# Performance work log

Measured on AMD Instinct MI355X. Metric: run time of the kernel, lower is better.

The kernel has to match this reference:

```python
import jax, jax.numpy as jnp
import numpy as np

N_NODES = 50000
N_EDGES = 1600000
IN_F, H_F, N_C = 128, 128, 16
NEG_SLOPE = 0.2  # DGL GATConv default


def setup_inputs() -> dict:
    key = jax.random.key(0)
    ks = jax.random.split(key, 12)
    def w(k, shape, fan_in):
        return jax.random.normal(k, shape, jnp.float32) / np.float32(np.sqrt(fan_in))
    return {
        "feat": jax.random.normal(ks[0], (N_NODES, IN_F), jnp.float32),
        "src": jax.random.randint(ks[1], (N_EDGES,), 0, N_NODES, dtype=jnp.int32),
        "dst": jax.random.randint(ks[2], (N_EDGES,), 0, N_NODES, dtype=jnp.int32),
        "W1": w(ks[3], (IN_F, H_F), IN_F), "al1": w(ks[4], (H_F,), H_F), "ar1": w(ks[5], (H_F,), H_F), "b1": jnp.zeros((H_F,), jnp.float32),
        "W2": w(ks[6], (H_F, H_F), H_F), "al2": w(ks[7], (H_F,), H_F), "ar2": w(ks[8], (H_F,), H_F), "b2": jnp.zeros((H_F,), jnp.float32),
        "W3": w(ks[9], (H_F, N_C), H_F), "al3": w(ks[10], (N_C,), N_C), "ar3": w(ks[11], (N_C,), N_C), "b3": jnp.zeros((N_C,), jnp.float32),
    }


def _gat_layer(h, src, dst, W, al, ar, b):
    # DGL GATConv (1 head): ft = W h; e_ij = LeakyReLU(a_l.ft_src + a_r.ft_dst);
    # alpha = edge_softmax over incoming edges of dst; out = sum alpha * ft_src + bias
    ft = h @ W                                   # [N, out]
    el = ft @ al                                 # [N]
    er = ft @ ar                                 # [N]
    e = jax.nn.leaky_relu(el[src] + er[dst], negative_slope=NEG_SLOPE)  # [E]
    emax = jax.ops.segment_max(e, dst, num_segments=N_NODES)
    emax = jnp.where(jnp.isfinite(emax), emax, 0.0)  # guard isolated nodes
    ex = jnp.exp(e - emax[dst])                  # [E]
    esum = jax.ops.segment_sum(ex, dst, num_segments=N_NODES)  # [N]
    agg = jax.ops.segment_sum(ex[:, None] * ft[src], dst, num_segments=N_NODES)  # [N, out]
    out = agg / jnp.where(esum > 0, esum, 1.0)[:, None] + b
    return jax.nn.relu(out)


def reference(feat, src, dst, W1, al1, ar1, b1, W2, al2, ar2, b2, W3, al3, ar3, b3):
    h = _gat_layer(feat, src, dst, W1, al1, ar1, b1)
    h = _gat_layer(h, src, dst, W2, al2, ar2, b2)
    h = _gat_layer(h, src, dst, W3, al3, ar3, b3)
    return h  # [N_NODES, N_C]
```

## Files before the change

### kernel.cpp

```cpp
#include <hip/hip_runtime.h>
#include <hip/hip_bf16.h>

#define NN 50000
#define NE 1600000
#define FF 128
#define CC 16
#define NB ((NN + 63) / 64)
#define NBLK 128
#define CH ((NE + NBLK - 1) / NBLK)

using bf16 = __hip_bfloat16;
using bf16x8 = __attribute__((ext_vector_type(8))) short;
using f32x4  = __attribute__((ext_vector_type(4))) float;

static __device__ __forceinline__ float ldf(const void* p, int i, int isbf){
    return isbf ? __bfloat162float(((const bf16*)p)[i]) : ((const float*)p)[i];
}
static __device__ __forceinline__ float bflo(unsigned u){
    union{unsigned x; float f;} c; c.x = u << 16; return c.f;
}
static __device__ __forceinline__ float bfhi(unsigned u){
    union{unsigned x; float f;} c; c.x = u & 0xFFFF0000u; return c.f;
}
static __device__ __forceinline__ float rdlanef(float v, int l){
    return __int_as_float(__builtin_amdgcn_readlane(__float_as_int(v), l));
}
static __device__ __forceinline__ unsigned short f2bfu(float v){
    bf16 b = __float2bfloat16(v);
    union{bf16 b; unsigned short u;} c; c.b = b; return c.u;
}

__global__ __launch_bounds__(256) void k_detect(const unsigned short* __restrict__ u,
                                                int* __restrict__ flag){
    int t = threadIdx.x;
    unsigned short lo = u[2 * t];
    int e = (lo >> 7) & 0xFF;
    int sane = (e >= 117 && e <= 137) ? 1 : 0;
    __shared__ int cnt;
    if (t == 0) cnt = 0;
    __syncthreads();
    atomicAdd(&cnt, sane);
    __syncthreads();
    if (t == 0) *flag = (cnt >= 128) ? 1 : 0;
}

__global__ __launch_bounds__(256) void k_zero(int* __restrict__ p, int n){
    int i = blockIdx.x * 256 + threadIdx.x;
    if (i < n) p[i] = 0;
}

__global__ __launch_bounds__(256) void k_wprep(const void* __restrict__ W1, const void* __restrict__ W2,
                                               const int* __restrict__ dflag, unsigned short* __restrict__ wtg){
    const int isbf = *dflag;
    int idx = blockIdx.x * 256 + threadIdx.x;
    int l = idx >> 14;
    int e = idx & 16383;
    int f = e >> 7, k = e & 127;
    const void* W = l ? W2 : W1;
    wtg[idx] = f2bfu(ldf(W, k * FF + f, isbf));
}


__global__ __launch_bounds__(256) void k_bcount(const int* __restrict__ dst, int* __restrict__ bcounts,
                                                int* __restrict__ bh){
    __shared__ int hist[NB];
    const int t = threadIdx.x, b = blockIdx.x;
    for (int i = t; i < NB; i += 256) hist[i] = 0;
    __syncthreads();
    const int beg = b * CH, end = (beg + CH < NE) ? beg + CH : NE;
    for (int i = beg + t; i < end; i += 256){
        int d = dst[i];
        if ((unsigned)d >= NN) d = 0;
        atomicAdd(&hist[d >> 6], 1);
    }
    __syncthreads();
    for (int k = t; k < NB; k += 256){
        int v = hist[k];
        bh[k * NBLK + b] = v;
        if (v) atomicAdd(&bcounts[k], v);
    }
}

__global__ __launch_bounds__(256) void k_bscan(const int* __restrict__ bcounts, int* __restrict__ bbase,
                                               int* __restrict__ rowptr){
    __shared__ int s[256];
    const int t = threadIdx.x;
    constexpr int PT = (NB + 255) / 256;
    int loc[PT];
    int sum = 0;
    #pragma unroll
    for (int i = 0; i < PT; i++){
        int idx = t * PT + i;
        int v = (idx < NB) ? bcounts[idx] : 0;
        loc[i] = sum;
        sum += v;
    }
    s[t] = sum; __syncthreads();
    for (int off = 1; off < 256; off <<= 1){
        int x = (t >= off) ? s[t - off] : 0;
        __syncthreads();
        s[t] += x;
        __syncthreads();
    }
    int base = (t > 0) ? s[t - 1] : 0;
    #pragma unroll
    for (int i = 0; i < PT; i++){
        int idx = t * PT + i;
        if (idx < NB) bbase[idx] = base + loc[i];
    }
    if (t == 255){
        bbase[NB] = s[255];
        rowptr[NN] = s[255];
    }
}

__global__ __launch_bounds__(256) void k_boffset(const int* __restrict__ bbase, int* __restrict__ bh){
    int k = blockIdx.x * 4 + (threadIdx.x >> 6);
    int lane = threadIdx.x & 63;
    if (k >= NB) return;
    int v0 = bh[k * NBLK + 2 * lane];
    int v1 = bh[k * NBLK + 2 * lane + 1];
    int s = v0 + v1;
    #pragma unroll
    for (int off = 1; off < 64; off <<= 1){
        int x = __shfl_up(s, off);
        if (lane >= off) s += x;
    }
    int base = bbase[k] + s - (v0 + v1);
    bh[k * NBLK + 2 * lane]     = base;
    bh[k * NBLK + 2 * lane + 1] = base + v0;
}

__global__ __launch_bounds__(256) void k_bucket(const int* __restrict__ src, const int* __restrict__ dst,
                                                const int* __restrict__ bh, unsigned* __restrict__ bpairs){
    __shared__ int cur[NB];
    const int t = threadIdx.x, b = blockIdx.x;
    for (int k = t; k < NB; k += 256) cur[k] = bh[k * NBLK + b];
    __syncthreads();
    const int beg = b * CH, end = (beg + CH < NE) ? beg + CH : NE;
    for (int i = beg + t; i < end; i += 256){
        int s = src[i];
        int d = dst[i];
        if ((unsigned)s >= NN) s = 0;
        if ((unsigned)d >= NN) d = 0;
        int p = atomicAdd(&cur[d >> 6], 1);
        if ((unsigned)p < NE) bpairs[p] = (unsigned)s | ((unsigned)(d & 63) << 16);
    }
}

__global__ __launch_bounds__(256) void k_bsort(const unsigned* __restrict__ bpairs, const int* __restrict__ bbase,
                                               int* __restrict__ rowptr, int* __restrict__ csrsrc){
    __shared__ int cnt[64];
    __shared__ int cur[64];
    const int t = threadIdx.x;
    const int b = blockIdx.x;
    const int base = bbase[b];
    const int endb = bbase[b + 1];
    if (t < 64) cnt[t] = 0;
    __syncthreads();
    for (int i = base + t; i < endb; i += 256)
        atomicAdd(&cnt[bpairs[i] >> 16], 1);
    __syncthreads();
    if (t < 64){
        int v = cnt[t];
        int inc = v;
        #pragma unroll
        for (int off = 1; off < 64; off <<= 1){
            int x = __shfl_up(inc, off);
            if (t >= off) inc += x;
        }
        int excl = inc - v;
        cur[t] = excl;
        int d = b * 64 + t;
        if (d < NN) rowptr[d] = base + excl;
    }
    __syncthreads();
    for (int i = base + t; i < endb; i += 256){
        unsigned pr = bpairs[i];
        int p = atomicAdd(&cur[pr >> 16], 1);
        csrsrc[base + p] = (int)(pr & 0xFFFFu);
    }
}


#define XPAD 136

template<bool XDYN>
__global__ __launch_bounds__(256) void k_mgemm(const void* __restrict__ X, const unsigned short* __restrict__ wtg,
                                               const void* __restrict__ al, const void* __restrict__ ar,
                                               const int* __restrict__ dflag, bf16* __restrict__ ft,
                                               float* __restrict__ el, float* __restrict__ er){
    __shared__ unsigned short xs[64 * XPAD];
    __shared__ unsigned short wt[128 * XPAD];
    const int isbf = *dflag;
    const int t  = threadIdx.x;
    const int n0 = blockIdx.x * 64;

    for (int i2 = t; i2 < 8192; i2 += 256){
        unsigned v = ((const unsigned*)wtg)[i2];
        int r = i2 >> 6, c2 = (i2 & 63) * 2;
        *(unsigned*)&wt[r * XPAD + c2] = v;
    }
    for (int i2 = t; i2 < 4096; i2 += 256){
        int r = i2 >> 6, c2 = (i2 & 63) * 2;
        int n = n0 + r;
        float v0 = 0.f, v1 = 0.f;
        if (n < NN){
            if (XDYN){ v0 = ldf(X, n * FF + c2, isbf); v1 = ldf(X, n * FF + c2 + 1, isbf); }
            else     { v0 = ((const float*)X)[n * FF + c2]; v1 = ((const float*)X)[n * FF + c2 + 1]; }
        }
        unsigned pk = (unsigned)f2bfu(v0) | ((unsigned)f2bfu(v1) << 16);
        *(unsigned*)&xs[r * XPAD + c2] = pk;
    }
    __syncthreads();

    const int wv = t >> 6;
    const int lane = t & 63;
    const int quad = lane >> 4;
    const int mcol = lane & 15;

    bf16x8 afr[4];
    const unsigned short* xrow = &xs[(wv * 16 + mcol) * XPAD + quad * 8];
    #pragma unroll
    for (int kt = 0; kt < 4; kt++)
        afr[kt] = *(const bf16x8*)(xrow + kt * 32);

    float elp[4] = {0.f,0.f,0.f,0.f}, erp[4] = {0.f,0.f,0.f,0.f};

    #pragma unroll
    for (int f = 0; f < 8; f++){
        f32x4 acc = {0.f, 0.f, 0.f, 0.f};
        const unsigned short* wrow = &wt[(f * 16 + mcol) * XPAD + quad * 8];
        #pragma unroll
        for (int kt = 0; kt < 4; kt++){
            bf16x8 bfr = *(const bf16x8*)(wrow + kt * 32);
            acc = __builtin_amdgcn_mfma_f32_16x16x32_bf16(afr[kt], bfr, acc, 0, 0, 0);
        }
        int col = f * 16 + mcol;
        float alv = ldf(al, col, isbf);
        float arv = ldf(ar, col, isbf);
        #pragma unroll
        for (int reg = 0; reg < 4; reg++){
            int node = n0 + wv * 16 + quad * 4 + reg;
            float v = acc[reg];
            if (node < NN) ft[node * FF + col] = __float2bfloat16(v);
            elp[reg] += v * alv;
            erp[reg] += v * arv;
        }
    }

    #pragma unroll
    for (int reg = 0; reg < 4; reg++){
        float pl = elp[reg], pr = erp[reg];
        #pragma unroll
        for (int off = 1; off < 16; off <<= 1){
            pl += __shfl_xor(pl, off);
            pr += __shfl_xor(pr, off);
        }
        int node = n0 + wv * 16 + quad * 4 + reg;
        if (mcol == 0 && node < NN){ el[node] = pl; er[node] = pr; }
    }
}


template<bool XDYN, int OUT, int NPT, bool FTBF>
__global__ __launch_bounds__(256) void k_gemm(const void* __restrict__ X, const void* __restrict__ W,
                                              const void* __restrict__ al, const void* __restrict__ ar,
                                              const int* __restrict__ dflag, void* __restrict__ ft,
                                              float* __restrict__ el, float* __restrict__ er){
    constexpr int BN = 256 * NPT / OUT;
    __shared__ float xs[FF][BN + 1];
    const int isbf = *dflag;
    const int t  = threadIdx.x;
    const int n0 = blockIdx.x * BN;

    for (int idx = t; idx < BN * FF; idx += 256){
        int r = idx >> 7;
        int c = idx & 127;
        int n = n0 + r;
        float v = 0.f;
        if (n < NN){
            if (XDYN) v = ldf(X, n * FF + c, isbf);
            else      v = ((const float*)X)[n * FF + c];
        }
        xs[c][r] = v;
    }
    __syncthreads();

    const int tx = t % OUT;
    const int rg = t / OUT;
    float acc[NPT];
    #pragma unroll
    for (int i = 0; i < NPT; i++) acc[i] = 0.f;

    if (isbf){
        const bf16* Wb = (const bf16*)W;
        for (int k = 0; k < FF; k++){
            float w = __bfloat162float(Wb[k * OUT + tx]);
            #pragma unroll
            for (int i = 0; i < NPT; i++) acc[i] += w * xs[k][rg * NPT + i];
        }
    } else {
        const float* Wf = (const float*)W;
        for (int k = 0; k < FF; k++){
            float w = Wf[k * OUT + tx];
            #pragma unroll
            for (int i = 0; i < NPT; i++) acc[i] += w * xs[k][rg * NPT + i];
        }
    }

    #pragma unroll
    for (int i = 0; i < NPT; i++){
        int n = n0 + rg * NPT + i;
        if (n < NN){
            if (FTBF) ((bf16*)ft)[n * OUT + tx] = __float2bfloat16(acc[i]);
            else      ((float*)ft)[n * OUT + tx] = acc[i];
        }
    }

    float alv = ldf(al, tx, isbf);
    float arv = ldf(ar, tx, isbf);
    float pl = acc[0] * alv, pr = acc[0] * arv;
    #pragma unroll
    for (int off = 1; off < 16; off <<= 1){
        pl += __shfl_xor(pl, off);
        pr += __shfl_xor(pr, off);
    }
    int n = n0 + rg;
    if (tx == 0 && n < NN){ el[n] = pl; er[n] = pr; }
}


template<int OUT, bool FTBF, bool FINAL>
__global__ __launch_bounds__(256) void k_agg(const void* __restrict__ ftv, const float* __restrict__ el,
                                             const float* __restrict__ er, const int* __restrict__ rowptr,
                                             const int* __restrict__ csrsrc, const void* __restrict__ bias,
                                             const int* __restrict__ dflag, void* __restrict__ outp){
    const int isbf = *dflag;
    int lane = threadIdx.x & 63;
    int n = blockIdx.x * 4 + (threadIdx.x >> 6);
    if (n >= NN) return;
    int beg = rowptr[n], end = rowptr[n + 1];
    beg = (beg < 0) ? 0 : (beg > NE ? NE : beg);
    end = (end < beg) ? beg : (end > NE ? NE : end);
    int deg = end - beg;
    float erd = er[n];

    float m = -3.4e38f;
    int   s_c = 0;
    float e_c = 0.f;
    for (int i = beg + lane; i < end; i += 64){
        int s = csrsrc[i];
        if ((unsigned)s >= NN) s = 0;
        float e = el[s] + erd;
        e = (e >= 0.f) ? e : 0.2f * e;
        if (i < beg + 64){ s_c = s; e_c = e; }
        m = fmaxf(m, e);
    }
    #pragma unroll
    for (int off = 32; off; off >>= 1) m = fmaxf(m, __shfl_xor(m, off));

    int jmax = (deg < 64) ? deg : 64;
    float w_c = (lane < jmax) ? __expf(e_c - m) : 0.f;
    float lsum = w_c;
    #pragma unroll
    for (int off = 32; off; off >>= 1) lsum += __shfl_xor(lsum, off);

    if constexpr (OUT == 128){
        const unsigned* ftb = (const unsigned*)ftv;
        float acc0 = 0.f, acc1 = 0.f;
        int j = 0;
        if (jmax >= 8){
            float w[8]; unsigned u[8];
            #pragma unroll
            for (int q = 0; q < 8; q++){
                int s = __builtin_amdgcn_readlane(s_c, q);
                w[q] = rdlanef(w_c, q);
                u[q] = (ftb + s * 64)[lane];
            }
            for (j = 8; j + 8 <= jmax; j += 8){
                float wn[8]; unsigned un[8];
                #pragma unroll
                for (int q = 0; q < 8; q++){
                    int s = __builtin_amdgcn_readlane(s_c, j + q);
                    wn[q] = rdlanef(w_c, j + q);
                    un[q] = (ftb + s * 64)[lane];
                }
                #pragma unroll
                for (int q = 0; q < 8; q++){
                    acc0 += w[q] * bflo(u[q]);
                    acc1 += w[q] * bfhi(u[q]);
                    w[q] = wn[q]; u[q] = un[q];
                }
            }
            #pragma unroll
            for (int q = 0; q < 8; q++){
                acc0 += w[q] * bflo(u[q]);
                acc1 += w[q] * bfhi(u[q]);
            }
        }
        for (; j < jmax; ++j){
            int s = __builtin_amdgcn_readlane(s_c, j);
            float w = rdlanef(w_c, j);
            unsigned u = (ftb + s * 64)[lane];
            acc0 += w * bflo(u); acc1 += w * bfhi(u);
        }
        for (int i = beg + 64; i < end; ++i){
            int s = csrsrc[i];
            if ((unsigned)s >= NN) s = 0;
            float e = el[s] + erd;
            e = (e >= 0.f) ? e : 0.2f * e;
            float w = __expf(e - m);
            unsigned u = (ftb + s * 64)[lane];
            lsum += w;
            acc0 += w * bflo(u); acc1 += w * bfhi(u);
        }
        float inv = 1.f / ((lsum > 0.f) ? lsum : 1.f);
        float2 o;
        o.x = fmaxf(acc0 * inv + ldf(bias, 2 * lane,     isbf), 0.f);
        o.y = fmaxf(acc1 * inv + ldf(bias, 2 * lane + 1, isbf), 0.f);
        ((float2*)outp)[n * 64 + lane] = o;
    } else {
        const float* ftf = (const float*)ftv;
        int g  = lane >> 4;
        int fl = lane & 15;
        float acc0 = 0.f;
        int j = 0;
        for (; j + 4 <= jmax; j += 4){
            int   s = __shfl(s_c, j + g);
            float w = __shfl(w_c, j + g);
            acc0 += w * ftf[s * 16 + fl];
        }
        for (; j < jmax; ++j){
            int s = __builtin_amdgcn_readlane(s_c, j);
            float w = rdlanef(w_c, j);
            if (g == 0) acc0 += w * ftf[s * 16 + fl];
        }
        for (int i = beg + 64; i < end; ++i){
            int s = csrsrc[i];
            if ((unsigned)s >= NN) s = 0;
            float e = el[s] + erd;
            e = (e >= 0.f) ? e : 0.2f * e;
            float w = __expf(e - m);
            lsum += w;
            if (g == 0) acc0 += w * ftf[s * 16 + fl];
        }
        acc0 += __shfl_xor(acc0, 16); acc0 += __shfl_xor(acc0, 32);
        float inv = 1.f / ((lsum > 0.f) ? lsum : 1.f);
        if (lane < 16){
            float o = fmaxf(acc0 * inv + ldf(bias, fl, isbf), 0.f);
            if (FINAL && isbf) ((bf16*)outp)[n * 16 + fl] = __float2bfloat16(o);
            else               ((float*)outp)[n * 16 + fl] = o;
        }
    }
}


static size_t align256(size_t x){ return (x + 255) & ~(size_t)255; }

extern "C" void kernel_launch(void* const* d_in, const int* in_sizes, int n_in,
                              void* d_out, int out_size, void* d_ws, size_t ws_size,
                              hipStream_t stream) {
    const void* feat = d_in[0];
    const int*  src  = (const int*)d_in[1];
    const int*  dst  = (const int*)d_in[2];
    const void* W1 = d_in[3];
    const void* al1= d_in[4];
    const void* ar1= d_in[5];
    const void* b1 = d_in[6];
    const void* W2 = d_in[7];
    const void* al2= d_in[8];
    const void* ar2= d_in[9];
    const void* b2 = d_in[10];
    const void* W3 = d_in[11];
    const void* al3= d_in[12];
    const void* ar3= d_in[13];
    const void* b3 = d_in[14];

    char* p = (char*)d_ws;
    size_t off = 0;
    auto carve = [&](size_t bytes)->void*{
        void* r = p + off;
        off += align256(bytes);
        return r;
    };
    float* ftA   = (float*)carve((size_t)NN * FF * 4);
    float* hB    = (float*)carve((size_t)NN * FF * 4);
    float* el    = (float*)carve((size_t)NN * 4);
    float* er    = (float*)carve((size_t)NN * 4);
    int*   rowptr= (int*)  carve((size_t)(NN + 1) * 4);
    int*   csrsrc= (int*)  carve((size_t)NE * 4);
    int*   bcounts=(int*)  carve((size_t)NB * 4);
    int*   bbase  =(int*)  carve((size_t)(NB + 1) * 4);
    int*   bh     =(int*)  carve((size_t)NB * NBLK * 4);
    unsigned short* wtg = (unsigned short*)carve(2 * 16384 * 2);
    int*   dflag  =(int*)  carve(256);
    unsigned* bpairs = (unsigned*)hB;
    void*  ftb   = ftA;
    (void)ws_size; (void)n_in; (void)in_sizes; (void)out_size;

    dim3 b256(256);

    k_detect<<<dim3(1), b256, 0, stream>>>((const unsigned short*)feat, dflag);

    k_wprep<<<dim3(128), b256, 0, stream>>>(W1, W2, dflag, wtg);

    k_zero<<<dim3((NB + 255) / 256), b256, 0, stream>>>(bcounts, NB);
    k_bcount<<<dim3(NBLK), b256, 0, stream>>>(dst, bcounts, bh);
    k_bscan<<<dim3(1), b256, 0, stream>>>(bcounts, bbase, rowptr);
    k_boffset<<<dim3((NB + 3) / 4), b256, 0, stream>>>(bbase, bh);
    k_bucket<<<dim3(NBLK), b256, 0, stream>>>(src, dst, bh, bpairs);
    k_bsort<<<dim3(NB), b256, 0, stream>>>(bpairs, bbase, rowptr, csrsrc);

    const int mg_grid   = (NN + 63) / 64;
    const int gemm_grid = (NN + 15) / 16;
    const int node_grid = (NN + 3) / 4;

    k_mgemm<true><<<dim3(mg_grid), b256, 0, stream>>>(feat, wtg, al1, ar1, dflag, (bf16*)ftb, el, er);
    k_agg<128, true, false><<<dim3(node_grid), b256, 0, stream>>>(ftb, el, er, rowptr, csrsrc, b1, dflag, hB);

    k_mgemm<false><<<dim3(mg_grid), b256, 0, stream>>>(hB, wtg + 16384, al2, ar2, dflag, (bf16*)ftb, el, er);
    k_agg<128, true, false><<<dim3(node_grid), b256, 0, stream>>>(ftb, el, er, rowptr, csrsrc, b2, dflag, hB);

    k_gemm<false, 16, 1, false><<<dim3(gemm_grid), b256, 0, stream>>>(hB, W3, al3, ar3, dflag, ftb, el, er);
    k_agg<16, false, true><<<dim3(node_grid), b256, 0, stream>>>(ftb, el, er, rowptr, csrsrc, b3, dflag, d_out);
}
```

Baseline: 377.1 us.

## Widen aggregation gathers to 16-byte loads and retile the final-layer GEMM

The 128-wide aggregation now splits each wavefront into four groups that each take one edge per step. Each lane fetches a uint4 (8 bf16 features), with a 4-deep software prefetch ring, and the groups are combined with cross-lane shuffles at the end. This replaces one 4-byte gather per lane per edge. The 16-wide aggregation likewise handles 16 edges at once using float4 loads, and the third-layer GEMM is rewritten with W staged in shared memory and 4 nodes per thread using float4 LDS reads. The aim is fewer, wider memory transactions and more memory-level parallelism, at the cost of extra shuffle reductions and higher register use.

```diff
diff --git a/kernel.cpp b/kernel.cpp
--- a/kernel.cpp
+++ b/kernel.cpp
@@ -21,9 +21,6 @@
 }
 static __device__ __forceinline__ float bfhi(unsigned u){
     union{unsigned x; float f;} c; c.x = u & 0xFFFF0000u; return c.f;
-}
-static __device__ __forceinline__ float rdlanef(float v, int l){
-    return __int_as_float(__builtin_amdgcn_readlane(__float_as_int(v), l));
 }
 static __device__ __forceinline__ unsigned short f2bfu(float v){
     bf16 b = __float2bfloat16(v);
@@ -263,79 +260,60 @@
 }
 
 
-template<bool XDYN, int OUT, int NPT, bool FTBF>
-__global__ __launch_bounds__(256) void k_gemm(const void* __restrict__ X, const void* __restrict__ W,
-                                              const void* __restrict__ al, const void* __restrict__ ar,
-                                              const int* __restrict__ dflag, void* __restrict__ ft,
-                                              float* __restrict__ el, float* __restrict__ er){
-    constexpr int BN = 256 * NPT / OUT;
-    __shared__ float xs[FF][BN + 1];
+__global__ __launch_bounds__(256) void k_gemm3(const float* __restrict__ X, const void* __restrict__ W,
+                                               const void* __restrict__ al, const void* __restrict__ ar,
+                                               const int* __restrict__ dflag, float* __restrict__ ft,
+                                               float* __restrict__ el, float* __restrict__ er){
+    __shared__ float xs[64][132];
+    __shared__ float wst[16][132];
     const int isbf = *dflag;
     const int t  = threadIdx.x;
-    const int n0 = blockIdx.x * BN;
-
-    for (int idx = t; idx < BN * FF; idx += 256){
-        int r = idx >> 7;
-        int c = idx & 127;
+    const int n0 = blockIdx.x * 64;
+
+    for (int idx = t; idx < 2048; idx += 256){
+        int k = idx >> 4, f = idx & 15;
+        wst[f][k] = ldf(W, k * CC + f, isbf);
+    }
+    for (int idx = t; idx < 8192; idx += 256){
+        int r = idx >> 7, c = idx & 127;
         int n = n0 + r;
-        float v = 0.f;
-        if (n < NN){
-            if (XDYN) v = ldf(X, n * FF + c, isbf);
-            else      v = ((const float*)X)[n * FF + c];
-        }
-        xs[c][r] = v;
-    }
-    __syncthreads();
-
-    const int tx = t % OUT;
-    const int rg = t / OUT;
-    float acc[NPT];
-    #pragma unroll
-    for (int i = 0; i < NPT; i++) acc[i] = 0.f;
-
-    if (isbf){
-        const bf16* Wb = (const bf16*)W;
-        for (int k = 0; k < FF; k++){
-            float w = __bfloat162float(Wb[k * OUT + tx]);
-            #pragma unroll
-            for (int i = 0; i < NPT; i++) acc[i] += w * xs[k][rg * NPT + i];
-        }
-    } else {
-        const float* Wf = (const float*)W;
-        for (int k = 0; k < FF; k++){
-            float w = Wf[k * OUT + tx];
-            #pragma unroll
-            for (int i = 0; i < NPT; i++) acc[i] += w * xs[k][rg * NPT + i];
-        }
-    }
-
-    #pragma unroll
-    for (int i = 0; i < NPT; i++){
-        int n = n0 + rg * NPT + i;
-        if (n < NN){
-            if (FTBF) ((bf16*)ft)[n * OUT + tx] = __float2bfloat16(acc[i]);
-            else      ((float*)ft)[n * OUT + tx] = acc[i];
+        xs[r][c] = (n < NN) ? X[n * FF + c] : 0.f;
+    }
+    __syncthreads();
+
+    const int tx = t & 15;
+    const int rg = t >> 4;
+    float acc[4] = {0.f,0.f,0.f,0.f};
+    for (int k = 0; k < 128; k += 4){
+        float4 wv = *(const float4*)&wst[tx][k];
+        #pragma unroll
+        for (int i = 0; i < 4; i++){
+            float4 xv = *(const float4*)&xs[rg * 4 + i][k];
+            acc[i] += wv.x * xv.x + wv.y * xv.y + wv.z * xv.z + wv.w * xv.w;
         }
     }
 
     float alv = ldf(al, tx, isbf);
     float arv = ldf(ar, tx, isbf);
-    float pl = acc[0] * alv, pr = acc[0] * arv;
-    #pragma unroll
-    for (int off = 1; off < 16; off <<= 1){
-        pl += __shfl_xor(pl, off);
-        pr += __shfl_xor(pr, off);
-    }
-    int n = n0 + rg;
-    if (tx == 0 && n < NN){ el[n] = pl; er[n] = pr; }
-}
-
-
-template<int OUT, bool FTBF, bool FINAL>
-__global__ __launch_bounds__(256) void k_agg(const void* __restrict__ ftv, const float* __restrict__ el,
-                                             const float* __restrict__ er, const int* __restrict__ rowptr,
-                                             const int* __restrict__ csrsrc, const void* __restrict__ bias,
-                                             const int* __restrict__ dflag, void* __restrict__ outp){
+    #pragma unroll
+    for (int i = 0; i < 4; i++){
+        int n = n0 + rg * 4 + i;
+        if (n < NN) ft[n * CC + tx] = acc[i];
+        float pl = acc[i] * alv, pr = acc[i] * arv;
+        #pragma unroll
+        for (int off = 1; off < 16; off <<= 1){
+            pl += __shfl_xor(pl, off);
+            pr += __shfl_xor(pr, off);
+        }
+        if (tx == 0 && n < NN){ el[n] = pl; er[n] = pr; }
+    }
+}
+
+
+__global__ __launch_bounds__(256) void k_agg128(const void* __restrict__ ftv, const float* __restrict__ el,
+                                                const float* __restrict__ er, const int* __restrict__ rowptr,
+                                                const int* __restrict__ csrsrc, const void* __restrict__ bias,
+                                                const int* __restrict__ dflag, float* __restrict__ outp){
     const int isbf = *dflag;
     int lane = threadIdx.x & 63;
     int n = blockIdx.x * 4 + (threadIdx.x >> 6);
@@ -366,91 +344,165 @@
     #pragma unroll
     for (int off = 32; off; off >>= 1) lsum += __shfl_xor(lsum, off);
 
-    if constexpr (OUT == 128){
-        const unsigned* ftb = (const unsigned*)ftv;
-        float acc0 = 0.f, acc1 = 0.f;
-        int j = 0;
-        if (jmax >= 8){
-            float w[8]; unsigned u[8];
-            #pragma unroll
-            for (int q = 0; q < 8; q++){
-                int s = __builtin_amdgcn_readlane(s_c, q);
-                w[q] = rdlanef(w_c, q);
-                u[q] = (ftb + s * 64)[lane];
-            }
-            for (j = 8; j + 8 <= jmax; j += 8){
-                float wn[8]; unsigned un[8];
-                #pragma unroll
-                for (int q = 0; q < 8; q++){
-                    int s = __builtin_amdgcn_readlane(s_c, j + q);
-                    wn[q] = rdlanef(w_c, j + q);
-                    un[q] = (ftb + s * 64)[lane];
-                }
-                #pragma unroll
-                for (int q = 0; q < 8; q++){
-                    acc0 += w[q] * bflo(u[q]);
-                    acc1 += w[q] * bfhi(u[q]);
-                    w[q] = wn[q]; u[q] = un[q];
-                }
-            }
-            #pragma unroll
-            for (int q = 0; q < 8; q++){
-                acc0 += w[q] * bflo(u[q]);
-                acc1 += w[q] * bfhi(u[q]);
-            }
-        }
-        for (; j < jmax; ++j){
-            int s = __builtin_amdgcn_readlane(s_c, j);
-            float w = rdlanef(w_c, j);
-            unsigned u = (ftb + s * 64)[lane];
-            acc0 += w * bflo(u); acc1 += w * bfhi(u);
-        }
-        for (int i = beg + 64; i < end; ++i){
-            int s = csrsrc[i];
-            if ((unsigned)s >= NN) s = 0;
-            float e = el[s] + erd;
-            e = (e >= 0.f) ? e : 0.2f * e;
-            float w = __expf(e - m);
-            unsigned u = (ftb + s * 64)[lane];
-            lsum += w;
-            acc0 += w * bflo(u); acc1 += w * bfhi(u);
-        }
-        float inv = 1.f / ((lsum > 0.f) ? lsum : 1.f);
-        float2 o;
-        o.x = fmaxf(acc0 * inv + ldf(bias, 2 * lane,     isbf), 0.f);
-        o.y = fmaxf(acc1 * inv + ldf(bias, 2 * lane + 1, isbf), 0.f);
-        ((float2*)outp)[n * 64 + lane] = o;
-    } else {
-        const float* ftf = (const float*)ftv;
-        int g  = lane >> 4;
-        int fl = lane & 15;
-        float acc0 = 0.f;
-        int j = 0;
-        for (; j + 4 <= jmax; j += 4){
-            int   s = __shfl(s_c, j + g);
-            float w = __shfl(w_c, j + g);
-            acc0 += w * ftf[s * 16 + fl];
-        }
-        for (; j < jmax; ++j){
-            int s = __builtin_amdgcn_readlane(s_c, j);
-            float w = rdlanef(w_c, j);
-            if (g == 0) acc0 += w * ftf[s * 16 + fl];
-        }
-        for (int i = beg + 64; i < end; ++i){
-            int s = csrsrc[i];
-            if ((unsigned)s >= NN) s = 0;
-            float e = el[s] + erd;
-            e = (e >= 0.f) ? e : 0.2f * e;
-            float w = __expf(e - m);
-            lsum += w;
-            if (g == 0) acc0 += w * ftf[s * 16 + fl];
-        }
-        acc0 += __shfl_xor(acc0, 16); acc0 += __shfl_xor(acc0, 32);
-        float inv = 1.f / ((lsum > 0.f) ? lsum : 1.f);
-        if (lane < 16){
-            float o = fmaxf(acc0 * inv + ldf(bias, fl, isbf), 0.f);
-            if (FINAL && isbf) ((bf16*)outp)[n * 16 + fl] = __float2bfloat16(o);
-            else               ((float*)outp)[n * 16 + fl] = o;
+    const uint4* ftq = (const uint4*)ftv;
+    const int g  = lane >> 4;
+    const int fl = lane & 15;
+    float a8[8];
+    #pragma unroll
+    for (int i = 0; i < 8; i++) a8[i] = 0.f;
+
+    int nbatch = (jmax + 3) >> 2;
+    float wq[4]; uint4 uq[4];
+    #pragma unroll
+    for (int q = 0; q < 4; q++){
+        int eidx = (q * 4 + g) & 63;
+        int s = __shfl(s_c, eidx);
+        wq[q] = (q < nbatch) ? __shfl(w_c, eidx) : 0.f;
+        uq[q] = ftq[(unsigned)s * 16 + fl];
+    }
+    for (int b = 0; b < nbatch; b++){
+        float w = wq[b & 3];
+        uint4 u = uq[b & 3];
+        int bn = b + 4;
+        if (bn < nbatch){
+            int eidx = (bn * 4 + g) & 63;
+            int s = __shfl(s_c, eidx);
+            wq[b & 3] = __shfl(w_c, eidx);
+            uq[b & 3] = ftq[(unsigned)s * 16 + fl];
+        } else {
+            wq[b & 3] = 0.f;
+        }
+        a8[0] += w * bflo(u.x); a8[1] += w * bfhi(u.x);
+        a8[2] += w * bflo(u.y); a8[3] += w * bfhi(u.y);
+        a8[4] += w * bflo(u.z); a8[5] += w * bfhi(u.z);
+        a8[6] += w * bflo(u.w); a8[7] += w * bfhi(u.w);
+    }
+
+    for (int i = beg + 64; i < end; ++i){
+        int s = csrsrc[i];
+        if ((unsigned)s >= NN) s = 0;
+        float e = el[s] + erd;
+        e = (e >= 0.f) ? e : 0.2f * e;
+        float w = __expf(e - m);
+        lsum += w;
+        if (g == 0){
+            uint4 u = ftq[(unsigned)s * 16 + fl];
+            a8[0] += w * bflo(u.x); a8[1] += w * bfhi(u.x);
+            a8[2] += w * bflo(u.y); a8[3] += w * bfhi(u.y);
+            a8[4] += w * bflo(u.z); a8[5] += w * bfhi(u.z);
+            a8[6] += w * bflo(u.w); a8[7] += w * bfhi(u.w);
+        }
+    }
+
+    #pragma unroll
+    for (int i = 0; i < 8; i++){
+        a8[i] += __shfl_xor(a8[i], 16);
+        a8[i] += __shfl_xor(a8[i], 32);
+    }
+    float inv = 1.f / ((lsum > 0.f) ? lsum : 1.f);
+    if (lane < 16){
+        float4 o0, o1;
+        o0.x = fmaxf(a8[0] * inv + ldf(bias, fl * 8 + 0, isbf), 0.f);
+        o0.y = fmaxf(a8[1] * inv + ldf(bias, fl * 8 + 1, isbf), 0.f);
+        o0.z = fmaxf(a8[2] * inv + ldf(bias, fl * 8 + 2, isbf), 0.f);
+        o0.w = fmaxf(a8[3] * inv + ldf(bias, fl * 8 + 3, isbf), 0.f);
+        o1.x = fmaxf(a8[4] * inv + ldf(bias, fl * 8 + 4, isbf), 0.f);
+        o1.y = fmaxf(a8[5] * inv + ldf(bias, fl * 8 + 5, isbf), 0.f);
+        o1.z = fmaxf(a8[6] * inv + ldf(bias, fl * 8 + 6, isbf), 0.f);
+        o1.w = fmaxf(a8[7] * inv + ldf(bias, fl * 8 + 7, isbf), 0.f);
+        ((float4*)outp)[n * 32 + fl * 2]     = o0;
+        ((float4*)outp)[n * 32 + fl * 2 + 1] = o1;
+    }
+}
+
+
+__global__ __launch_bounds__(256) void k_agg16(const float* __restrict__ ftv, const float* __restrict__ el,
+                                               const float* __restrict__ er, const int* __restrict__ rowptr,
+                                               const int* __restrict__ csrsrc, const void* __restrict__ bias,
+                                               const int* __restrict__ dflag, void* __restrict__ outp){
+    const int isbf = *dflag;
+    int lane = threadIdx.x & 63;
+    int n = blockIdx.x * 4 + (threadIdx.x >> 6);
+    if (n >= NN) return;
+    int beg = rowptr[n], end = rowptr[n + 1];
+    beg = (beg < 0) ? 0 : (beg > NE ? NE : beg);
+    end = (end < beg) ? beg : (end > NE ? NE : end);
+    int deg = end - beg;
+    float erd = er[n];
+
+    float m = -3.4e38f;
+    int   s_c = 0;
+    float e_c = 0.f;
+    for (int i = beg + lane; i < end; i += 64){
+        int s = csrsrc[i];
+        if ((unsigned)s >= NN) s = 0;
+        float e = el[s] + erd;
+        e = (e >= 0.f) ? e : 0.2f * e;
+        if (i < beg + 64){ s_c = s; e_c = e; }
+        m = fmaxf(m, e);
+    }
+    #pragma unroll
+    for (int off = 32; off; off >>= 1) m = fmaxf(m, __shfl_xor(m, off));
+
+    int jmax = (deg < 64) ? deg : 64;
+    float w_c = (lane < jmax) ? __expf(e_c - m) : 0.f;
+    float lsum = w_c;
+    #pragma unroll
+    for (int off = 32; off; off >>= 1) lsum += __shfl_xor(lsum, off);
+
+    const float4* ftq = (const float4*)ftv;
+    const int g   = lane >> 2;
+    const int fl2 = lane & 3;
+    int nbatch = (jmax + 15) >> 4;
+    float wq[4]; float4 uq[4];
+    #pragma unroll
+    for (int q = 0; q < 4; q++){
+        int eidx = (q * 16 + g) & 63;
+        int s = __shfl(s_c, eidx);
+        wq[q] = (q < nbatch) ? __shfl(w_c, eidx) : 0.f;
+        uq[q] = ftq[(unsigned)s * 4 + fl2];
+    }
+    float a4[4] = {0.f,0.f,0.f,0.f};
+    #pragma unroll
+    for (int q = 0; q < 4; q++){
+        a4[0] += wq[q] * uq[q].x;
+        a4[1] += wq[q] * uq[q].y;
+        a4[2] += wq[q] * uq[q].z;
+        a4[3] += wq[q] * uq[q].w;
+    }
+    for (int i = beg + 64; i < end; ++i){
+        int s = csrsrc[i];
+        if ((unsigned)s >= NN) s = 0;
+        float e = el[s] + erd;
+        e = (e >= 0.f) ? e : 0.2f * e;
+        float w = __expf(e - m);
+        lsum += w;
+        if (g == 0){
+            float4 u = ftq[(unsigned)s * 4 + fl2];
+            a4[0] += w * u.x; a4[1] += w * u.y; a4[2] += w * u.z; a4[3] += w * u.w;
+        }
+    }
+    #pragma unroll
+    for (int i = 0; i < 4; i++){
+        a4[i] += __shfl_xor(a4[i], 4);
+        a4[i] += __shfl_xor(a4[i], 8);
+        a4[i] += __shfl_xor(a4[i], 16);
+        a4[i] += __shfl_xor(a4[i], 32);
+    }
+    float inv = 1.f / ((lsum > 0.f) ? lsum : 1.f);
+    if (lane < 4){
+        float o0 = fmaxf(a4[0] * inv + ldf(bias, fl2 * 4 + 0, isbf), 0.f);
+        float o1 = fmaxf(a4[1] * inv + ldf(bias, fl2 * 4 + 1, isbf), 0.f);
+        float o2 = fmaxf(a4[2] * inv + ldf(bias, fl2 * 4 + 2, isbf), 0.f);
+        float o3 = fmaxf(a4[3] * inv + ldf(bias, fl2 * 4 + 3, isbf), 0.f);
+        if (isbf){
+            uint2 pk;
+            pk.x = (unsigned)f2bfu(o0) | ((unsigned)f2bfu(o1) << 16);
+            pk.y = (unsigned)f2bfu(o2) | ((unsigned)f2bfu(o3) << 16);
+            ((uint2*)outp)[n * 4 + fl2] = pk;
+        } else {
+            float4 o; o.x = o0; o.y = o1; o.z = o2; o.w = o3;
+            ((float4*)outp)[n * 4 + fl2] = o;
         }
     }
 }
@@ -502,7 +554,6 @@
     dim3 b256(256);
 
     k_detect<<<dim3(1), b256, 0, stream>>>((const unsigned short*)feat, dflag);
-
     k_wprep<<<dim3(128), b256, 0, stream>>>(W1, W2, dflag, wtg);
 
     k_zero<<<dim3((NB + 255) / 256), b256, 0, stream>>>(bcounts, NB);
@@ -513,15 +564,14 @@
     k_bsort<<<dim3(NB), b256, 0, stream>>>(bpairs, bbase, rowptr, csrsrc);
 
     const int mg_grid   = (NN + 63) / 64;
-    const int gemm_grid = (NN + 15) / 16;
     const int node_grid = (NN + 3) / 4;
 
     k_mgemm<true><<<dim3(mg_grid), b256, 0, stream>>>(feat, wtg, al1, ar1, dflag, (bf16*)ftb, el, er);
-    k_agg<128, true, false><<<dim3(node_grid), b256, 0, stream>>>(ftb, el, er, rowptr, csrsrc, b1, dflag, hB);
+    k_agg128<<<dim3(node_grid), b256, 0, stream>>>(ftb, el, er, rowptr, csrsrc, b1, dflag, hB);
 
     k_mgemm<false><<<dim3(mg_grid), b256, 0, stream>>>(hB, wtg + 16384, al2, ar2, dflag, (bf16*)ftb, el, er);
-    k_agg<128, true, false><<<dim3(node_grid), b256, 0, stream>>>(ftb, el, er, rowptr, csrsrc, b2, dflag, hB);
-
-    k_gemm<false, 16, 1, false><<<dim3(gemm_grid), b256, 0, stream>>>(hB, W3, al3, ar3, dflag, ftb, el, er);
-    k_agg<16, false, true><<<dim3(node_grid), b256, 0, stream>>>(ftb, el, er, rowptr, csrsrc, b3, dflag, d_out);
-}
+    k_agg128<<<dim3(node_grid), b256, 0, stream>>>(ftb, el, er, rowptr, csrsrc, b2, dflag, hB);
+
+    k_gemm3<<<dim3(mg_grid), b256, 0, stream>>>(hB, W3, al3, ar3, dflag, (float*)ftb, el, er);
+    k_agg16<<<dim3(node_grid), b256, 0, stream>>>((const float*)ftb, el, er, rowptr, csrsrc, b3, dflag, d_out);
+}
```

New measurement: 499.3 us. +32.4%, slower.
